# Performance work log

Measured on AMD Instinct MI355X. Metric: run time of the kernel, lower is better.

The kernel has to match this reference:

```python
import jax, jax.numpy as jnp
import numpy as np

DIM = 224
HEADS = 8
DH = 28
WS = 8
INNER = DH * HEADS  # 224
SCALE = DH ** -0.5
B, H, W = 256, 32, 32


def setup_inputs() -> dict:
    key = jax.random.key(0)
    ks = jax.random.split(key, 6)
    x = jax.random.normal(ks[0], (B, H, W, DIM), jnp.float32)
    Wq = jax.random.normal(ks[1], (DIM, INNER), jnp.float32) * 0.02
    Wkv = jax.random.normal(ks[2], (DIM, 2 * INNER), jnp.float32) * 0.02
    Wo = jax.random.normal(ks[3], (INNER, DIM), jnp.float32) * 0.02
    bo = jnp.zeros((DIM,), jnp.float32)
    seq_l1 = WS * WS                      # 64 tokens per window
    hw = 256 // HEADS                     # 32
    seq_l2 = hw * hw // seq_l1            # 16 windows
    pos_emb1 = jax.random.normal(ks[4], (1, 1, HEADS // 2, seq_l1, seq_l1), jnp.float32)
    pos_emb2 = jax.random.normal(ks[5], (1, 1, HEADS // 2, seq_l2, seq_l2), jnp.float32)
    return {"x": x, "Wq": Wq, "Wkv": Wkv, "Wo": Wo, "bo": bo,
            "pos_emb1": pos_emb1, "pos_emb2": pos_emb2}


def _win_part(t):
    # [b, H, W, c] -> [b, n_windows, WS*WS, c]
    b, h, w, c = t.shape
    t = t.reshape(b, h // WS, WS, w // WS, WS, c).transpose(0, 1, 3, 2, 4, 5)
    return t.reshape(b, (h // WS) * (w // WS), WS * WS, c)


def _win_merge(t, h, w):
    # [b, n_windows, WS*WS, c] -> [b, H, W, c]
    b, n, mm, c = t.shape
    t = t.reshape(b, h // WS, w // WS, WS, WS, c).transpose(0, 1, 3, 2, 4, 5)
    return t.reshape(b, h, w, c)


def _attn(q, k, v, pos):
    # q,k,v: [b, n, mm, ch]; split into HEADS//2 heads of dim d
    b, n, mm, ch = q.shape
    hh = HEADS // 2
    d = ch // hh
    def sp(t):
        return t.reshape(b, n, mm, hh, d).transpose(0, 1, 3, 2, 4)  # [b,n,hh,mm,d]
    q, k, v = sp(q) * SCALE, sp(k), sp(v)
    sim = jnp.einsum('bnhid,bnhjd->bnhij', q, k) + pos
    sim = jnp.roll(sim, (1, 1), axis=(3, 4))
    attn = jax.nn.softmax(sim, axis=-1)
    o = jnp.einsum('bnhij,bnhjd->bnhid', attn, v)
    return o.transpose(0, 1, 3, 2, 4).reshape(b, n, mm, ch)


def reference(x, Wq, Wkv, Wo, bo, pos_emb1, pos_emb2):
    b, h, w, c = x.shape
    q = x @ Wq
    kv = x @ Wkv
    k, v = kv[..., :INNER], kv[..., INNER:]
    half = c // 2
    # Branch 1: local attention within each 8x8 window (first half of channels)
    q1, k1, v1 = (_win_part(t[..., :half]) for t in (q, k, v))
    out1 = _attn(q1, k1, v1, pos_emb1)  # [b, n, mm, half]
    # Branch 2: attention across windows at same intra-window position (second half)
    q2, k2, v2 = (_win_part(t[..., half:]).transpose(0, 2, 1, 3) for t in (q, k, v))
    out2 = _attn(q2, k2, v2, pos_emb2).transpose(0, 2, 1, 3)  # [b, n, mm, half]
    out = jnp.concatenate([out1, out2], axis=-1) @ Wo + bo
    return _win_merge(out, h, w)
```

## Files before the change

### kernel.cpp

```cpp
#include <hip/hip_runtime.h>

typedef __bf16 bf16_t;
typedef __bf16 bf16x4 __attribute__((ext_vector_type(4)));
typedef __bf16 bf16x8 __attribute__((ext_vector_type(8)));
typedef float  f32x4  __attribute__((ext_vector_type(4)));

#define MFMA16(a, b, c) __builtin_amdgcn_mfma_f32_16x16x32_bf16((a), (b), (c), 0, 0, 0)

#define ATT_SCALE 0.1889822365046136f

__device__ __forceinline__ bf16x8 load8_masked(const bf16_t* p, bool full) {
  bf16x4 lo = *reinterpret_cast<const bf16x4*>(p);
  bf16x4 hi = {};
  if (full) hi = *reinterpret_cast<const bf16x4*>(p + 4);
  bf16x8 r;
  r[0] = lo[0]; r[1] = lo[1]; r[2] = lo[2]; r[3] = lo[3];
  r[4] = hi[0]; r[5] = hi[1]; r[6] = hi[2]; r[7] = hi[3];
  return r;
}

__global__ __launch_bounds__(256) void prep_w(
    const float* __restrict__ Wq, const float* __restrict__ Wkv,
    const float* __restrict__ Wo,
    bf16_t* __restrict__ wqt, bf16_t* __restrict__ wkvt, bf16_t* __restrict__ wot) {
  const int id = blockIdx.x * 256 + threadIdx.x;
  if (id < 224 * 224) {
    const int n = id / 224, kk = id % 224;
    wqt[id] = (bf16_t)Wq[kk * 224 + n];
  } else if (id < 224 * 224 + 448 * 224) {
    const int t = id - 224 * 224;
    const int n = t / 224, kk = t % 224;
    wkvt[t] = (bf16_t)Wkv[kk * 448 + n];
  } else {
    const int t = id - (224 * 224 + 448 * 224);
    const int n = t / 224, kk = t % 224;
    wot[t] = (bf16_t)Wo[kk * 224 + n];
  }
}

__global__ __launch_bounds__(256) void qkv_gemm(
    const float* __restrict__ x, const bf16_t* __restrict__ wqt,
    const bf16_t* __restrict__ wkvt,
    bf16_t* __restrict__ q, bf16_t* __restrict__ k, bf16_t* __restrict__ v) {
  __shared__ bf16_t xs[128][240];
  __shared__ bf16_t wls[224][40];
  const int tid = threadIdx.x;
  const int blk = blockIdx.x;
  {
    const int b = blk >> 3;
    for (int idx = tid; idx < 128 * 56; idx += 256) {
      const int r = idx / 56, c4 = idx % 56;
      const int win = ((blk & 7) << 1) | (r >> 6);
      const int p = r & 63;
      const int hh = ((win >> 2) << 3) | (p >> 3);
      const int ww = ((win & 3) << 3) | (p & 7);
      const float4 f = *reinterpret_cast<const float4*>(
          x + (size_t)((b * 32 + hh) * 32 + ww) * 224 + c4 * 4);
      bf16x4 o;
      o[0] = (bf16_t)f.x; o[1] = (bf16_t)f.y; o[2] = (bf16_t)f.z; o[3] = (bf16_t)f.w;
      *reinterpret_cast<bf16x4*>(&xs[r][c4 * 4]) = o;
    }
  }
  const int lane = tid & 63;
  const int col = lane & 15, g = lane >> 4;
  const int wid = tid >> 6;
  const int wr = wid >> 1, wc = wid & 1;
  const f32x4 vzero = {0.f, 0.f, 0.f, 0.f};
  __syncthreads();
  for (int chunk = 0; chunk < 3; ++chunk) {
    const bf16_t* wt = (chunk == 0) ? wqt : ((chunk == 1) ? wkvt : (wkvt + 224 * 224));
    bf16_t* dst = (chunk == 0) ? q : ((chunk == 1) ? k : v);
    f32x4 acc[4][7];
#pragma unroll
    for (int ti = 0; ti < 4; ++ti)
#pragma unroll
      for (int tj = 0; tj < 7; ++tj) acc[ti][tj] = vzero;
    for (int ks = 0; ks < 7; ++ks) {
      for (int idx = tid; idx < 224 * 4; idx += 256) {
        const int n = idx >> 2, part = idx & 3;
        *reinterpret_cast<uint4*>(&wls[n][part * 8]) =
            *reinterpret_cast<const uint4*>(wt + n * 224 + ks * 32 + part * 8);
      }
      __syncthreads();
      bf16x8 af[4];
#pragma unroll
      for (int ti = 0; ti < 4; ++ti)
        af[ti] = *reinterpret_cast<const bf16x8*>(&xs[wr * 64 + ti * 16 + col][ks * 32 + g * 8]);
#pragma unroll
      for (int tj = 0; tj < 7; ++tj) {
        const bf16x8 bfr = *reinterpret_cast<const bf16x8*>(&wls[wc * 112 + tj * 16 + col][g * 8]);
#pragma unroll
        for (int ti = 0; ti < 4; ++ti)
          acc[ti][tj] = MFMA16(af[ti], bfr, acc[ti][tj]);
      }
      __syncthreads();
    }
    const size_t base = (size_t)blk * 128;
#pragma unroll
    for (int ti = 0; ti < 4; ++ti)
#pragma unroll
      for (int tj = 0; tj < 7; ++tj)
#pragma unroll
        for (int r = 0; r < 4; ++r) {
          const int row = wr * 64 + ti * 16 + g * 4 + r;
          const int cn = wc * 112 + tj * 16 + col;
          dst[(base + row) * 224 + cn] = (bf16_t)acc[ti][tj][r];
        }
  }
}

__global__ __launch_bounds__(256) void attn1(
    const bf16_t* __restrict__ q, const bf16_t* __restrict__ k,
    const bf16_t* __restrict__ v, const float* __restrict__ pos1,
    bf16_t* __restrict__ ao) {
  __shared__ bf16_t Vt[4][32][72];
  __shared__ bf16_t Pl[4][64][72];
  const int tid = threadIdx.x, blk = blockIdx.x;
  const int wid = tid >> 6, lane = tid & 63;
  const int col = lane & 15, g = lane >> 4;
  const size_t rowbase = (size_t)blk * 64;
  {
    const bf16_t* src = v + (rowbase + lane) * 224 + 28 * wid;
    const int j = (lane + 63) & 63;
#pragma unroll
    for (int c = 0; c < 28; c += 4) {
      const bf16x4 d = *reinterpret_cast<const bf16x4*>(src + c);
      Vt[wid][c + 0][j] = d[0]; Vt[wid][c + 1][j] = d[1];
      Vt[wid][c + 2][j] = d[2]; Vt[wid][c + 3][j] = d[3];
    }
#pragma unroll
    for (int c = 28; c < 32; ++c) Vt[wid][c][lane] = (bf16_t)0.f;
  }
  bf16x8 aQ[4], bK[4];
#pragma unroll
  for (int t = 0; t < 4; ++t) {
    const size_t off = (rowbase + t * 16 + col) * 224 + 28 * wid + 8 * g;
    aQ[t] = load8_masked(q + off, g < 3);
    bK[t] = load8_masked(k + off, g < 3);
  }
  const f32x4 vzero = {0.f, 0.f, 0.f, 0.f};
  f32x4 s[4][4];
#pragma unroll
  for (int ti = 0; ti < 4; ++ti)
#pragma unroll
    for (int tj = 0; tj < 4; ++tj)
      s[ti][tj] = MFMA16(aQ[ti], bK[tj], vzero);
  const float* pe = pos1 + wid * 4096;
#pragma unroll
  for (int ti = 0; ti < 4; ++ti)
#pragma unroll
    for (int tj = 0; tj < 4; ++tj)
#pragma unroll
      for (int r = 0; r < 4; ++r)
        s[ti][tj][r] = s[ti][tj][r] * ATT_SCALE +
                       pe[(ti * 16 + g * 4 + r) * 64 + tj * 16 + col];
#pragma unroll
  for (int ti = 0; ti < 4; ++ti) {
#pragma unroll
    for (int r = 0; r < 4; ++r) {
      float m = fmaxf(fmaxf(s[ti][0][r], s[ti][1][r]), fmaxf(s[ti][2][r], s[ti][3][r]));
#pragma unroll
      for (int d = 1; d < 16; d <<= 1) m = fmaxf(m, __shfl_xor(m, d));
      float sum = 0.f;
#pragma unroll
      for (int tj = 0; tj < 4; ++tj) {
        const float e = __expf(s[ti][tj][r] - m);
        s[ti][tj][r] = e; sum += e;
      }
#pragma unroll
      for (int d = 1; d < 16; d <<= 1) sum += __shfl_xor(sum, d);
      const float inv = 1.f / sum;
#pragma unroll
      for (int tj = 0; tj < 4; ++tj) s[ti][tj][r] *= inv;
    }
  }
#pragma unroll
  for (int ti = 0; ti < 4; ++ti)
#pragma unroll
    for (int tj = 0; tj < 4; ++tj)
#pragma unroll
      for (int r = 0; r < 4; ++r)
        Pl[wid][ti * 16 + g * 4 + r][tj * 16 + col] = (bf16_t)s[ti][tj][r];
  __syncthreads();
#pragma unroll
  for (int ti = 0; ti < 4; ++ti)
#pragma unroll
    for (int t2 = 0; t2 < 2; ++t2) {
      f32x4 o = vzero;
#pragma unroll
      for (int ks = 0; ks < 2; ++ks) {
        const bf16x8 aP = *reinterpret_cast<const bf16x8*>(&Pl[wid][ti * 16 + col][ks * 32 + g * 8]);
        const bf16x8 bV = *reinterpret_cast<const bf16x8*>(&Vt[wid][t2 * 16 + col][ks * 32 + g * 8]);
        o = MFMA16(aP, bV, o);
      }
      const int ch = t2 * 16 + col;
      if (ch < 28) {
#pragma unroll
        for (int r = 0; r < 4; ++r) {
          const int i = ti * 16 + g * 4 + r;
          ao[(rowbase + ((i + 1) & 63)) * 224 + 28 * wid + ch] = (bf16_t)o[r];
        }
      }
    }
}

__global__ __launch_bounds__(256) void attn2(
    const bf16_t* __restrict__ q, const bf16_t* __restrict__ k,
    const bf16_t* __restrict__ v, const float* __restrict__ pos2,
    bf16_t* __restrict__ ao) {
  __shared__ bf16_t Vt2[4][32][40];
  __shared__ bf16_t P2[4][16][40];
  const int tid = threadIdx.x, blk = blockIdx.x;
  const int wid = tid >> 6, lane = tid & 63;
  const int col = lane & 15, g = lane >> 4;
  const int b = blk >> 4;
  const int pos = (blk & 15) * 4 + wid;
  {
    unsigned short* z1 = reinterpret_cast<unsigned short*>(&Vt2[wid][0][0]);
    for (int i = lane; i < 32 * 40; i += 64) z1[i] = 0;
    unsigned short* z2 = reinterpret_cast<unsigned short*>(&P2[wid][0][0]);
    for (int i = lane; i < 16 * 40; i += 64) z2[i] = 0;
  }
  __syncthreads();
  const f32x4 vzero = {0.f, 0.f, 0.f, 0.f};
  for (int h = 0; h < 4; ++h) {
    {
      const bf16_t* src = v + ((size_t)(b * 16 + col) * 64 + pos) * 224 + 112 + 28 * h + 7 * g;
      const int jd = (col + 15) & 15;
#pragma unroll
      for (int i = 0; i < 7; ++i) Vt2[wid][7 * g + i][jd] = src[i];
    }
    const size_t off = ((size_t)(b * 16 + col) * 64 + pos) * 224 + 112 + 28 * h + 8 * g;
    const bf16x8 aQ = load8_masked(q + off, g < 3);
    const bf16x8 bK = load8_masked(k + off, g < 3);
    f32x4 s = MFMA16(aQ, bK, vzero);
    const float* pe = pos2 + h * 256;
#pragma unroll
    for (int r = 0; r < 4; ++r)
      s[r] = s[r] * ATT_SCALE + pe[(g * 4 + r) * 16 + col];
#pragma unroll
    for (int r = 0; r < 4; ++r) {
      float m = s[r];
#pragma unroll
      for (int d = 1; d < 16; d <<= 1) m = fmaxf(m, __shfl_xor(m, d));
      const float e = __expf(s[r] - m);
      float sum = e;
#pragma unroll
      for (int d = 1; d < 16; d <<= 1) sum += __shfl_xor(sum, d);
      s[r] = e / sum;
    }
#pragma unroll
    for (int r = 0; r < 4; ++r) P2[wid][g * 4 + r][col] = (bf16_t)s[r];
    __syncthreads();
    const bf16x8 aP = *reinterpret_cast<const bf16x8*>(&P2[wid][col][g * 8]);
#pragma unroll
    for (int t2 = 0; t2 < 2; ++t2) {
      const bf16x8 bV = *reinterpret_cast<const bf16x8*>(&Vt2[wid][t2 * 16 + col][g * 8]);
      const f32x4 o = MFMA16(aP, bV, vzero);
      const int ch = t2 * 16 + col;
      if (ch < 28) {
#pragma unroll
        for (int r = 0; r < 4; ++r) {
          const int wo = ((g * 4 + r) + 1) & 15;
          ao[((size_t)(b * 16 + wo) * 64 + pos) * 224 + 112 + 28 * h + ch] = (bf16_t)o[r];
        }
      }
    }
    __syncthreads();
  }
}

__global__ __launch_bounds__(256) void out_gemm(
    const bf16_t* __restrict__ ao, const bf16_t* __restrict__ wot,
    const float* __restrict__ bo, float* __restrict__ out) {
  __shared__ bf16_t xs[128][240];
  __shared__ bf16_t wls[224][40];
  const int tid = threadIdx.x, blk = blockIdx.x;
  for (int idx = tid; idx < 128 * 28; idx += 256) {
    const int r = idx / 28, sg = idx % 28;
    *reinterpret_cast<uint4*>(&xs[r][sg * 8]) =
        *reinterpret_cast<const uint4*>(ao + ((size_t)blk * 128 + r) * 224 + sg * 8);
  }
  const int lane = tid & 63;
  const int col = lane & 15, g = lane >> 4;
  const int wid = tid >> 6;
  const int wr = wid >> 1, wc = wid & 1;
  const f32x4 vzero = {0.f, 0.f, 0.f, 0.f};
  f32x4 acc[4][7];
#pragma unroll
  for (int ti = 0; ti < 4; ++ti)
#pragma unroll
    for (int tj = 0; tj < 7; ++tj) acc[ti][tj] = vzero;
  __syncthreads();
  for (int ks = 0; ks < 7; ++ks) {
    for (int idx = tid; idx < 224 * 4; idx += 256) {
      const int n = idx >> 2, part = idx & 3;
      *reinterpret_cast<uint4*>(&wls[n][part * 8]) =
          *reinterpret_cast<const uint4*>(wot + n * 224 + ks * 32 + part * 8);
    }
    __syncthreads();
    bf16x8 af[4];
#pragma unroll
    for (int ti = 0; ti < 4; ++ti)
      af[ti] = *reinterpret_cast<const bf16x8*>(&xs[wr * 64 + ti * 16 + col][ks * 32 + g * 8]);
#pragma unroll
    for (int tj = 0; tj < 7; ++tj) {
      const bf16x8 bfr = *reinterpret_cast<const bf16x8*>(&wls[wc * 112 + tj * 16 + col][g * 8]);
#pragma unroll
      for (int ti = 0; ti < 4; ++ti)
        acc[ti][tj] = MFMA16(af[ti], bfr, acc[ti][tj]);
    }
    __syncthreads();
  }
  float bias[7];
#pragma unroll
  for (int tj = 0; tj < 7; ++tj) bias[tj] = bo[wc * 112 + tj * 16 + col];
  const int b = blk >> 3;
#pragma unroll
  for (int ti = 0; ti < 4; ++ti)
#pragma unroll
    for (int tj = 0; tj < 7; ++tj)
#pragma unroll
      for (int r = 0; r < 4; ++r) {
        const int row = wr * 64 + ti * 16 + g * 4 + r;
        const int cn = wc * 112 + tj * 16 + col;
        const int win = ((blk & 7) << 1) | (row >> 6);
        const int p = row & 63;
        const int hh = ((win >> 2) << 3) | (p >> 3);
        const int ww = ((win & 3) << 3) | (p & 7);
        out[(size_t)((b * 32 + hh) * 32 + ww) * 224 + cn] = acc[ti][tj][r] + bias[tj];
      }
}

extern "C" void kernel_launch(void* const* d_in, const int* in_sizes, int n_in,
                              void* d_out, int out_size, void* d_ws, size_t ws_size,
                              hipStream_t stream) {
  const float* x   = (const float*)d_in[0];
  const float* Wq  = (const float*)d_in[1];
  const float* Wkv = (const float*)d_in[2];
  const float* Wo  = (const float*)d_in[3];
  const float* bo  = (const float*)d_in[4];
  const float* p1  = (const float*)d_in[5];
  const float* p2  = (const float*)d_in[6];
  char* w = (char*)d_ws;
  bf16_t* q_ws  = (bf16_t*)(w);
  bf16_t* k_ws  = (bf16_t*)(w + 117440512);
  bf16_t* v_ws  = (bf16_t*)(w + 234881024);
  bf16_t* ao_ws = (bf16_t*)(w + 352321536);
  bf16_t* wqt   = (bf16_t*)(w + 469762048);
  bf16_t* wkvt  = (bf16_t*)(w + 469862400);
  bf16_t* wot   = (bf16_t*)(w + 470063104);

  prep_w<<<784, 256, 0, stream>>>(Wq, Wkv, Wo, wqt, wkvt, wot);
  qkv_gemm<<<2048, 256, 0, stream>>>(x, wqt, wkvt, q_ws, k_ws, v_ws);
  attn1<<<4096, 256, 0, stream>>>(q_ws, k_ws, v_ws, p1, ao_ws);
  attn2<<<4096, 256, 0, stream>>>(q_ws, k_ws, v_ws, p2, ao_ws);
  out_gemm<<<2048, 256, 0, stream>>>(ao_ws, wot, bo, (float*)d_out);
}
```

Measured before the change: 1.111 ms.

## Pre-swizzle weights into MFMA fragment layout and split GEMMs into smaller tiles

prep_w now writes the weights in a per-lane MFMA B-fragment order, so the GEMM kernels load B fragments straight from global memory (L2-resident) and no longer stage them through LDS or synchronise per k-step. The QKV GEMM is split so that each block handles one 64-row window and one of q/k/v, and out_gemm uses 64-row tiles. Occupancy hints of 4 blocks per CU are added. The cost is that each x tile is read three times (once per chunk) and there is less register-level reuse of B fragments.

```diff
diff --git a/kernel.cpp b/kernel.cpp
--- a/kernel.cpp
+++ b/kernel.cpp
@@ -22,91 +22,81 @@
 __global__ __launch_bounds__(256) void prep_w(
     const float* __restrict__ Wq, const float* __restrict__ Wkv,
     const float* __restrict__ Wo,
-    bf16_t* __restrict__ wqt, bf16_t* __restrict__ wkvt, bf16_t* __restrict__ wot) {
+    bf16_t* __restrict__ wsw_qkv, bf16_t* __restrict__ wsw_o) {
   const int id = blockIdx.x * 256 + threadIdx.x;
-  if (id < 224 * 224) {
-    const int n = id / 224, kk = id % 224;
-    wqt[id] = (bf16_t)Wq[kk * 224 + n];
-  } else if (id < 224 * 224 + 448 * 224) {
-    const int t = id - 224 * 224;
-    const int n = t / 224, kk = t % 224;
-    wkvt[t] = (bf16_t)Wkv[kk * 448 + n];
-  } else {
-    const int t = id - (224 * 224 + 448 * 224);
-    const int n = t / 224, kk = t % 224;
-    wot[t] = (bf16_t)Wo[kk * 224 + n];
-  }
-}
-
-__global__ __launch_bounds__(256) void qkv_gemm(
-    const float* __restrict__ x, const bf16_t* __restrict__ wqt,
-    const bf16_t* __restrict__ wkvt,
+  const int buf = id / 6272;
+  const int rem = id % 6272;
+  const int ks = rem / 896, rem2 = rem % 896;
+  const int nt = rem2 / 64, lane = rem2 % 64;
+  const int col = lane & 15, g = lane >> 4;
+  const int n = nt * 16 + col;
+  const int k0 = ks * 32 + g * 8;
+  const float* src;
+  int stride;
+  if (buf == 0)      { src = Wq + n;        stride = 224; }
+  else if (buf == 1) { src = Wkv + n;       stride = 448; }
+  else if (buf == 2) { src = Wkv + 224 + n; stride = 448; }
+  else               { src = Wo + n;        stride = 224; }
+  bf16x8 o;
+#pragma unroll
+  for (int e = 0; e < 8; ++e) o[e] = (bf16_t)src[(size_t)(k0 + e) * stride];
+  bf16_t* dst = (buf < 3) ? (wsw_qkv + buf * 100352) : wsw_o;
+  *reinterpret_cast<bf16x8*>(dst + ((ks * 14 + nt) * 64 + lane) * 8) = o;
+}
+
+__global__ __launch_bounds__(256, 4) void qkv_gemm(
+    const float* __restrict__ x, const bf16_t* __restrict__ wsw,
     bf16_t* __restrict__ q, bf16_t* __restrict__ k, bf16_t* __restrict__ v) {
-  __shared__ bf16_t xs[128][240];
-  __shared__ bf16_t wls[224][40];
+  __shared__ bf16_t xs[64][232];
   const int tid = threadIdx.x;
   const int blk = blockIdx.x;
-  {
-    const int b = blk >> 3;
-    for (int idx = tid; idx < 128 * 56; idx += 256) {
-      const int r = idx / 56, c4 = idx % 56;
-      const int win = ((blk & 7) << 1) | (r >> 6);
-      const int p = r & 63;
-      const int hh = ((win >> 2) << 3) | (p >> 3);
-      const int ww = ((win & 3) << 3) | (p & 7);
-      const float4 f = *reinterpret_cast<const float4*>(
-          x + (size_t)((b * 32 + hh) * 32 + ww) * 224 + c4 * 4);
-      bf16x4 o;
-      o[0] = (bf16_t)f.x; o[1] = (bf16_t)f.y; o[2] = (bf16_t)f.z; o[3] = (bf16_t)f.w;
-      *reinterpret_cast<bf16x4*>(&xs[r][c4 * 4]) = o;
-    }
-  }
-  const int lane = tid & 63;
-  const int col = lane & 15, g = lane >> 4;
-  const int wid = tid >> 6;
+  const int mt = blk / 3, chunk = blk % 3;
+  const int b = mt >> 4, win = mt & 15;
+  for (int idx = tid; idx < 64 * 56; idx += 256) {
+    const int r = idx / 56, c4 = idx % 56;
+    const int hh = ((win >> 2) << 3) | (r >> 3);
+    const int ww = ((win & 3) << 3) | (r & 7);
+    const float4 f = *reinterpret_cast<const float4*>(
+        x + (size_t)((b * 32 + hh) * 32 + ww) * 224 + c4 * 4);
+    bf16x4 o;
+    o[0] = (bf16_t)f.x; o[1] = (bf16_t)f.y; o[2] = (bf16_t)f.z; o[3] = (bf16_t)f.w;
+    *reinterpret_cast<bf16x4*>(&xs[r][c4 * 4]) = o;
+  }
+  const int lane = tid & 63, wid = tid >> 6;
+  const int col = lane & 15, g = lane >> 4;
   const int wr = wid >> 1, wc = wid & 1;
+  const bf16_t* wt = wsw + chunk * 100352;
+  bf16_t* dst = (chunk == 0) ? q : ((chunk == 1) ? k : v);
+  f32x4 acc[2][7];
   const f32x4 vzero = {0.f, 0.f, 0.f, 0.f};
+#pragma unroll
+  for (int ti = 0; ti < 2; ++ti)
+#pragma unroll
+    for (int tj = 0; tj < 7; ++tj) acc[ti][tj] = vzero;
   __syncthreads();
-  for (int chunk = 0; chunk < 3; ++chunk) {
-    const bf16_t* wt = (chunk == 0) ? wqt : ((chunk == 1) ? wkvt : (wkvt + 224 * 224));
-    bf16_t* dst = (chunk == 0) ? q : ((chunk == 1) ? k : v);
-    f32x4 acc[4][7];
-#pragma unroll
-    for (int ti = 0; ti < 4; ++ti)
-#pragma unroll
-      for (int tj = 0; tj < 7; ++tj) acc[ti][tj] = vzero;
-    for (int ks = 0; ks < 7; ++ks) {
-      for (int idx = tid; idx < 224 * 4; idx += 256) {
-        const int n = idx >> 2, part = idx & 3;
-        *reinterpret_cast<uint4*>(&wls[n][part * 8]) =
-            *reinterpret_cast<const uint4*>(wt + n * 224 + ks * 32 + part * 8);
-      }
-      __syncthreads();
-      bf16x8 af[4];
-#pragma unroll
-      for (int ti = 0; ti < 4; ++ti)
-        af[ti] = *reinterpret_cast<const bf16x8*>(&xs[wr * 64 + ti * 16 + col][ks * 32 + g * 8]);
-#pragma unroll
-      for (int tj = 0; tj < 7; ++tj) {
-        const bf16x8 bfr = *reinterpret_cast<const bf16x8*>(&wls[wc * 112 + tj * 16 + col][g * 8]);
-#pragma unroll
-        for (int ti = 0; ti < 4; ++ti)
-          acc[ti][tj] = MFMA16(af[ti], bfr, acc[ti][tj]);
-      }
-      __syncthreads();
-    }
-    const size_t base = (size_t)blk * 128;
-#pragma unroll
-    for (int ti = 0; ti < 4; ++ti)
-#pragma unroll
-      for (int tj = 0; tj < 7; ++tj)
-#pragma unroll
-        for (int r = 0; r < 4; ++r) {
-          const int row = wr * 64 + ti * 16 + g * 4 + r;
-          const int cn = wc * 112 + tj * 16 + col;
-          dst[(base + row) * 224 + cn] = (bf16_t)acc[ti][tj][r];
-        }
-  }
+#pragma unroll
+  for (int ks = 0; ks < 7; ++ks) {
+    bf16x8 af0 = *reinterpret_cast<const bf16x8*>(&xs[wr * 32 + col][ks * 32 + g * 8]);
+    bf16x8 af1 = *reinterpret_cast<const bf16x8*>(&xs[wr * 32 + 16 + col][ks * 32 + g * 8]);
+#pragma unroll
+    for (int tj = 0; tj < 7; ++tj) {
+      const bf16x8 bfr = *reinterpret_cast<const bf16x8*>(
+          wt + (((ks * 14) + wc * 7 + tj) * 64 + lane) * 8);
+      acc[0][tj] = MFMA16(af0, bfr, acc[0][tj]);
+      acc[1][tj] = MFMA16(af1, bfr, acc[1][tj]);
+    }
+  }
+  const size_t base = (size_t)mt * 64;
+#pragma unroll
+  for (int ti = 0; ti < 2; ++ti)
+#pragma unroll
+    for (int tj = 0; tj < 7; ++tj)
+#pragma unroll
+      for (int r = 0; r < 4; ++r) {
+        const int row = wr * 32 + ti * 16 + g * 4 + r;
+        const int cn = wc * 112 + tj * 16 + col;
+        dst[(base + row) * 224 + cn] = (bf16_t)acc[ti][tj][r];
+      }
 }
 
 __global__ __launch_bounds__(256) void attn1(
@@ -270,62 +260,50 @@
   }
 }
 
-__global__ __launch_bounds__(256) void out_gemm(
-    const bf16_t* __restrict__ ao, const bf16_t* __restrict__ wot,
+__global__ __launch_bounds__(256, 4) void out_gemm(
+    const bf16_t* __restrict__ ao, const bf16_t* __restrict__ wsw,
     const float* __restrict__ bo, float* __restrict__ out) {
-  __shared__ bf16_t xs[128][240];
-  __shared__ bf16_t wls[224][40];
+  __shared__ bf16_t xs[64][232];
   const int tid = threadIdx.x, blk = blockIdx.x;
-  for (int idx = tid; idx < 128 * 28; idx += 256) {
+  for (int idx = tid; idx < 64 * 28; idx += 256) {
     const int r = idx / 28, sg = idx % 28;
     *reinterpret_cast<uint4*>(&xs[r][sg * 8]) =
-        *reinterpret_cast<const uint4*>(ao + ((size_t)blk * 128 + r) * 224 + sg * 8);
-  }
-  const int lane = tid & 63;
-  const int col = lane & 15, g = lane >> 4;
-  const int wid = tid >> 6;
+        *reinterpret_cast<const uint4*>(ao + ((size_t)blk * 64 + r) * 224 + sg * 8);
+  }
+  const int lane = tid & 63, wid = tid >> 6;
+  const int col = lane & 15, g = lane >> 4;
   const int wr = wid >> 1, wc = wid & 1;
+  f32x4 acc[2][7];
   const f32x4 vzero = {0.f, 0.f, 0.f, 0.f};
-  f32x4 acc[4][7];
-#pragma unroll
-  for (int ti = 0; ti < 4; ++ti)
+#pragma unroll
+  for (int ti = 0; ti < 2; ++ti)
 #pragma unroll
     for (int tj = 0; tj < 7; ++tj) acc[ti][tj] = vzero;
   __syncthreads();
+#pragma unroll
   for (int ks = 0; ks < 7; ++ks) {
-    for (int idx = tid; idx < 224 * 4; idx += 256) {
-      const int n = idx >> 2, part = idx & 3;
-      *reinterpret_cast<uint4*>(&wls[n][part * 8]) =
-          *reinterpret_cast<const uint4*>(wot + n * 224 + ks * 32 + part * 8);
-    }
-    __syncthreads();
-    bf16x8 af[4];
-#pragma unroll
-    for (int ti = 0; ti < 4; ++ti)
-      af[ti] = *reinterpret_cast<const bf16x8*>(&xs[wr * 64 + ti * 16 + col][ks * 32 + g * 8]);
+    bf16x8 af0 = *reinterpret_cast<const bf16x8*>(&xs[wr * 32 + col][ks * 32 + g * 8]);
+    bf16x8 af1 = *reinterpret_cast<const bf16x8*>(&xs[wr * 32 + 16 + col][ks * 32 + g * 8]);
 #pragma unroll
     for (int tj = 0; tj < 7; ++tj) {
-      const bf16x8 bfr = *reinterpret_cast<const bf16x8*>(&wls[wc * 112 + tj * 16 + col][g * 8]);
-#pragma unroll
-      for (int ti = 0; ti < 4; ++ti)
-        acc[ti][tj] = MFMA16(af[ti], bfr, acc[ti][tj]);
-    }
-    __syncthreads();
+      const bf16x8 bfr = *reinterpret_cast<const bf16x8*>(
+          wsw + (((ks * 14) + wc * 7 + tj) * 64 + lane) * 8);
+      acc[0][tj] = MFMA16(af0, bfr, acc[0][tj]);
+      acc[1][tj] = MFMA16(af1, bfr, acc[1][tj]);
+    }
   }
   float bias[7];
 #pragma unroll
   for (int tj = 0; tj < 7; ++tj) bias[tj] = bo[wc * 112 + tj * 16 + col];
-  const int b = blk >> 3;
-#pragma unroll
-  for (int ti = 0; ti < 4; ++ti)
+  const int b = blk >> 4, win = blk & 15;
+#pragma unroll
+  for (int ti = 0; ti < 2; ++ti)
 #pragma unroll
     for (int tj = 0; tj < 7; ++tj)
 #pragma unroll
       for (int r = 0; r < 4; ++r) {
-        const int row = wr * 64 + ti * 16 + g * 4 + r;
+        const int p = wr * 32 + ti * 16 + g * 4 + r;
         const int cn = wc * 112 + tj * 16 + col;
-        const int win = ((blk & 7) << 1) | (row >> 6);
-        const int p = row & 63;
         const int hh = ((win >> 2) << 3) | (p >> 3);
         const int ww = ((win & 3) << 3) | (p & 7);
         out[(size_t)((b * 32 + hh) * 32 + ww) * 224 + cn] = acc[ti][tj][r] + bias[tj];
@@ -343,17 +321,16 @@
   const float* p1  = (const float*)d_in[5];
   const float* p2  = (const float*)d_in[6];
   char* w = (char*)d_ws;
-  bf16_t* q_ws  = (bf16_t*)(w);
-  bf16_t* k_ws  = (bf16_t*)(w + 117440512);
-  bf16_t* v_ws  = (bf16_t*)(w + 234881024);
-  bf16_t* ao_ws = (bf16_t*)(w + 352321536);
-  bf16_t* wqt   = (bf16_t*)(w + 469762048);
-  bf16_t* wkvt  = (bf16_t*)(w + 469862400);
-  bf16_t* wot   = (bf16_t*)(w + 470063104);
-
-  prep_w<<<784, 256, 0, stream>>>(Wq, Wkv, Wo, wqt, wkvt, wot);
-  qkv_gemm<<<2048, 256, 0, stream>>>(x, wqt, wkvt, q_ws, k_ws, v_ws);
+  bf16_t* q_ws    = (bf16_t*)(w);
+  bf16_t* k_ws    = (bf16_t*)(w + 117440512);
+  bf16_t* v_ws    = (bf16_t*)(w + 234881024);
+  bf16_t* ao_ws   = (bf16_t*)(w + 352321536);
+  bf16_t* wsw_qkv = (bf16_t*)(w + 469762048);
+  bf16_t* wsw_o   = (bf16_t*)(w + 470063104);
+
+  prep_w<<<98, 256, 0, stream>>>(Wq, Wkv, Wo, wsw_qkv, wsw_o);
+  qkv_gemm<<<12288, 256, 0, stream>>>(x, wsw_qkv, q_ws, k_ws, v_ws);
   attn1<<<4096, 256, 0, stream>>>(q_ws, k_ws, v_ws, p1, ao_ws);
   attn2<<<4096, 256, 0, stream>>>(q_ws, k_ws, v_ws, p2, ao_ws);
-  out_gemm<<<2048, 256, 0, stream>>>(ao_ws, wot, bo, (float*)d_out);
-}
+  out_gemm<<<4096, 256, 0, stream>>>(ao_ws, wsw_o, bo, (float*)d_out);
+}
```

After: 1.010 ms. 1.1x faster.
